# Optimization experiments

Hardware: AMD Instinct MI355X
Metric: run time of the kernel (lower is better)

The kernel has to match this reference:

```python
import jax, jax.numpy as jnp
import numpy as np

N_NODES = 100000
N_EDGES = 1600000
D = 64
L = 3


def setup_inputs() -> dict:
    key = jax.random.key(0)
    ks = jax.random.split(key, 6)
    x = jax.random.normal(ks[0], (N_NODES, D), dtype=jnp.float32)
    edge_index = jax.random.randint(ks[1], (2, N_EDGES), 0, N_NODES, dtype=jnp.int64)
    # Stacked SAGEConv params: lin_l (neighbor branch, with bias), lin_r (root branch, no bias)
    scale = 1.0 / np.sqrt(D)
    Wl = jax.random.normal(ks[2], (L, D, D), dtype=jnp.float32) * scale
    bl = jnp.zeros((L, D), dtype=jnp.float32)
    Wr = jax.random.normal(ks[3], (L, D, D), dtype=jnp.float32) * scale
    return {
        "x": x,
        "Wl": Wl,
        "bl": bl,
        "Wr": Wr,
        "edge_index": edge_index,
        "batch_size": N_NODES,
        "framework": 1,
    }


def reference(x, Wl, bl, Wr, edge_index, batch_size, framework):
    src, dst = edge_index[0], edge_index[1]
    n = x.shape[0]
    # in-degree for mean aggregation; isolated nodes -> divide by 1 (result stays 0)
    deg = jax.ops.segment_sum(jnp.ones((src.shape[0],), dtype=x.dtype), dst, num_segments=n)
    inv_deg = (1.0 / jnp.maximum(deg, 1.0))[:, None]  # [N,1]
    for i in range(Wl.shape[0]):
        msg = x[src]                                              # [E, D] gather
        agg = jax.ops.segment_sum(msg, dst, num_segments=n) * inv_deg  # [N, D] mean
        x = jax.nn.relu(agg @ Wl[i].T + bl[i] + x @ Wr[i].T)
    if framework:
        return x
    return x[:batch_size]
```

## Files before the change

kernel.cpp:

```cpp
#include <hip/hip_runtime.h>
#include <hip/hip_bf16.h>


#define D 64
#define KDIM 128
#define TS 64
#define ASTH 136
#define BSH 8
#define BNODES 256
#define ECHUNK 4096
#define BCAP 4864

typedef unsigned long long u64;
typedef unsigned short u16;
typedef __attribute__((ext_vector_type(8))) short bf16x8;
typedef __attribute__((ext_vector_type(4))) float f32x4;

__device__ inline u16 f2bf(float f) {
    unsigned u = __float_as_uint(f);
    return (u16)((u + 0x7fffu + ((u >> 16) & 1u)) >> 16);
}
__device__ inline void bfx8_to_f(uint4 u, float* f) {
    f[0] = __uint_as_float(u.x << 16); f[1] = __uint_as_float(u.x & 0xffff0000u);
    f[2] = __uint_as_float(u.y << 16); f[3] = __uint_as_float(u.y & 0xffff0000u);
    f[4] = __uint_as_float(u.z << 16); f[5] = __uint_as_float(u.z & 0xffff0000u);
    f[6] = __uint_as_float(u.w << 16); f[7] = __uint_as_float(u.w & 0xffff0000u);
}

__global__ __launch_bounds__(256) void setup_kernel(
    const float* __restrict__ x, u16* __restrict__ xb, int total8,
    const float* __restrict__ Wl, const float* __restrict__ Wr,
    u16* __restrict__ wpk, int wtotal)
{
    int gid = blockIdx.x * 256 + threadIdx.x;
    if (gid < total8) {
        float4 a = *(const float4*)(x + (size_t)gid * 8);
        float4 b = *(const float4*)(x + (size_t)gid * 8 + 4);
        uint4 o;
        o.x = (unsigned)f2bf(a.x) | ((unsigned)f2bf(a.y) << 16);
        o.y = (unsigned)f2bf(a.z) | ((unsigned)f2bf(a.w) << 16);
        o.z = (unsigned)f2bf(b.x) | ((unsigned)f2bf(b.y) << 16);
        o.w = (unsigned)f2bf(b.z) | ((unsigned)f2bf(b.w) << 16);
        *(uint4*)(xb + (size_t)gid * 8) = o;
    } else {
        int idx = gid - total8;
        if (idx < wtotal) {
            int j    = idx & 7;
            int lane = (idx >> 3) & 63;
            int nt   = (idx >> 9) & 3;
            int kt   = (idx >> 11) & 3;
            int l    = idx >> 13;
            int k = kt * 32 + (lane >> 4) * 8 + j;
            int n = nt * 16 + (lane & 15);
            float v = (k < D) ? Wl[((l * D) + n) * D + k]
                              : Wr[((l * D) + n) * D + (k - D)];
            wpk[idx] = f2bf(v);
        }
    }
}


__global__ __launch_bounds__(256) void bin_kernel(
    const int* __restrict__ srcp, const int* __restrict__ dstp,
    int* __restrict__ bcnt, u64* __restrict__ staging,
    int nE, int nb)
{
    __shared__ int hist[512];
    __shared__ int bbase[512];
    int t = threadIdx.x;
    int e0 = blockIdx.x * ECHUNK;
    for (int i = t; i < nb; i += 256) hist[i] = 0;
    __syncthreads();
    int dcache[16];
#pragma unroll
    for (int j = 0; j < 16; ++j) {
        int e = e0 + j * 256 + t;
        int d = (e < nE) ? dstp[e] : -1;
        dcache[j] = d;
        if (d >= 0) atomicAdd(&hist[d >> BSH], 1);
    }
    __syncthreads();
    for (int i = t; i < nb; i += 256) {
        int c = hist[i];
        bbase[i] = (c > 0) ? atomicAdd(&bcnt[i], c) : 0;
        hist[i] = 0;
    }
    __syncthreads();
#pragma unroll
    for (int j = 0; j < 16; ++j) {
        int e = e0 + j * 256 + t;
        int d = dcache[j];
        if (d >= 0) {
            int b = d >> BSH;
            int pos = bbase[b] + atomicAdd(&hist[b], 1);
            u64 rec = ((u64)(unsigned)(d & (BNODES - 1)) << 32) | (unsigned)srcp[e];
            staging[(size_t)b * BCAP + pos] = rec;
        }
    }
}

__global__ __launch_bounds__(256) void bucket_build_kernel(
    const u64* __restrict__ staging, const int* __restrict__ bcnt,
    int* __restrict__ offs, float* __restrict__ inv,
    int* __restrict__ csr, int n, int nb, int E)
{
    __shared__ int hist[BNODES];
    __shared__ int loffs[BNODES + 1];
    __shared__ int cur[BNODES];
    __shared__ int sbase;
    int b = blockIdx.x, t = threadIdx.x;
    int n0 = b << BSH;
    int nodes = min(BNODES, n - n0);
    int cnt = bcnt[b];
    const u64* seg = staging + (size_t)b * BCAP;
    if (t < 64) {
        int partial = 0;
        for (int i = t; i < b; i += 64) partial += bcnt[i];
#pragma unroll
        for (int off = 32; off > 0; off >>= 1) partial += __shfl_xor(partial, off);
        if (t == 0) sbase = partial;
    }
    for (int i = t; i < nodes; i += 256) { hist[i] = 0; cur[i] = 0; }
    __syncthreads();
    int gbase = sbase;
    for (int e = t; e < cnt; e += 256) atomicAdd(&hist[(int)(seg[e] >> 32)], 1);
    __syncthreads();
    if (t < 64) {
        int carry = 0;
        for (int base0 = 0; base0 < nodes; base0 += 64) {
            int i = base0 + t;
            int v = (i < nodes) ? hist[i] : 0;
            int inc = v;
#pragma unroll
            for (int off = 1; off < 64; off <<= 1) {
                int v2 = __shfl_up(inc, off);
                if (t >= off) inc += v2;
            }
            if (i < nodes) loffs[i] = carry + (inc - v);
            carry += __shfl(inc, 63);
        }
        if (t == 0) loffs[nodes] = carry;
    }
    __syncthreads();
    for (int i = t; i < nodes; i += 256) {
        offs[n0 + i] = gbase + loffs[i];
        inv[n0 + i] = 1.0f / fmaxf((float)hist[i], 1.0f);
    }
    if (b == nb - 1 && t == 0) offs[n] = E;
    for (int e = t; e < cnt; e += 256) {
        u64 rec = seg[e];
        int dl = (int)(rec >> 32);
        int sv = (int)(rec & 0xffffffffu);
        int pos = loffs[dl] + atomicAdd(&cur[dl], 1);
        csr[gbase + pos] = sv;
    }
}


template <int WRITE_F32>
__global__ __launch_bounds__(512, 6) void layer_kernel(
    const u16* __restrict__ xin, const int* __restrict__ offs,
    const int* __restrict__ csr, const float* __restrict__ inv,
    const u16* __restrict__ wpk,
    const float* __restrict__ bl,
    void* __restrict__ outp, int n)
{
    __shared__ u16 A[TS * ASTH];
    const int t = threadIdx.x, w = t >> 6, lane = t & 63;
    const int sub = lane >> 3;
    const int fl  = lane & 7;
    const int base = lane & 56;
    const int v0 = blockIdx.x * TS;

    const int r = w * 8 + sub;
    const int v = v0 + r;
    int s = 0, e = 0;
    float scale = 0.f;
    uint4 xv = make_uint4(0, 0, 0, 0);
    if (v < n) {
        s = offs[v];
        e = offs[v + 1];
        scale = inv[v];
        xv = *(const uint4*)(xin + (size_t)v * D + fl * 8);
    }
    float acc[8] = {};
    int idx = 0;
    if (s + fl < e) idx = csr[s + fl];
    while (__any(s < e)) {
        int cnt = e - s;
        cnt = cnt < 0 ? 0 : (cnt > 8 ? 8 : cnt);
        int idxv[8];
#pragma unroll
        for (int j = 0; j < 8; ++j) idxv[j] = __shfl(idx, base + j);
        uint4 rows[8];
#pragma unroll
        for (int j = 0; j < 8; ++j)
            rows[j] = *(const uint4*)(xin + (size_t)idxv[j] * D + fl * 8);
        int s2 = s + 8;
        idx = 0;
        if (s2 + fl < e) idx = csr[s2 + fl];
#pragma unroll
        for (int j = 0; j < 8; ++j) {
            float f[8];
            bfx8_to_f(rows[j], f);
            float m = (j < cnt) ? 1.f : 0.f;
#pragma unroll
            for (int q = 0; q < 8; ++q) acc[q] = fmaf(f[q], m, acc[q]);
        }
        s = s2;
    }
    uint4 o;
    o.x = (unsigned)f2bf(acc[0] * scale) | ((unsigned)f2bf(acc[1] * scale) << 16);
    o.y = (unsigned)f2bf(acc[2] * scale) | ((unsigned)f2bf(acc[3] * scale) << 16);
    o.z = (unsigned)f2bf(acc[4] * scale) | ((unsigned)f2bf(acc[5] * scale) << 16);
    o.w = (unsigned)f2bf(acc[6] * scale) | ((unsigned)f2bf(acc[7] * scale) << 16);
    *(uint4*)(&A[r * ASTH + fl * 8]) = o;
    *(uint4*)(&A[r * ASTH + D + fl * 8]) = xv;
    __syncthreads();

    const int m = lane & 15, quad = lane >> 4;
    const int row16 = (w >> 1) * 16;
    const int ntb = (w & 1) * 2;
    f32x4 cacc[2];
    cacc[0] = (f32x4){0.f, 0.f, 0.f, 0.f};
    cacc[1] = (f32x4){0.f, 0.f, 0.f, 0.f};
#pragma unroll
    for (int kt = 0; kt < 4; ++kt) {
        bf16x8 af = *(const bf16x8*)(&A[(row16 + m) * ASTH + kt * 32 + quad * 8]);
#pragma unroll
        for (int ntl = 0; ntl < 2; ++ntl) {
            bf16x8 bf = *(const bf16x8*)(wpk + (size_t)((kt * 4 + ntb + ntl) * 64 + lane) * 8);
            cacc[ntl] = __builtin_amdgcn_mfma_f32_16x16x32_bf16(af, bf, cacc[ntl], 0, 0, 0);
        }
    }
#pragma unroll
    for (int ntl = 0; ntl < 2; ++ntl) {
        int col = (ntb + ntl) * 16 + m;
        float bias = bl[col];
#pragma unroll
        for (int reg = 0; reg < 4; ++reg) {
            int row = row16 + quad * 4 + reg;
            int vv = v0 + row;
            if (vv < n) {
                float val = fmaxf(cacc[ntl][reg] + bias, 0.f);
                if (WRITE_F32)
                    ((float*)outp)[(size_t)vv * D + col] = val;
                else
                    ((u16*)outp)[(size_t)vv * D + col] = f2bf(val);
            }
        }
    }
}


extern "C" void kernel_launch(void* const* d_in, const int* in_sizes, int n_in,
                              void* d_out, int out_size, void* d_ws, size_t ws_size,
                              hipStream_t stream)
{
    const float* x  = (const float*)d_in[0];
    const float* Wl = (const float*)d_in[1];
    const float* bl = (const float*)d_in[2];
    const float* Wr = (const float*)d_in[3];
    const int*   ei = (const int*)d_in[4];

    const int N = in_sizes[0] / D;
    const int E = in_sizes[4] / 2;
    const int L = in_sizes[1] / (D * D);

    const int* srcp = ei;
    const int* dstp = ei + E;

    const int nbuck = (N + BNODES - 1) >> BSH;

    char* w = (char*)d_ws;
    int* bcnt  = (int*)w;               w += 512 * sizeof(int);
    int* offs  = (int*)w;               w += (size_t)(N + 1) * sizeof(int);
    w = (char*)(((uintptr_t)w + 15) & ~(uintptr_t)15);
    float* inv = (float*)w;             w += (size_t)N * sizeof(float);
    w = (char*)(((uintptr_t)w + 15) & ~(uintptr_t)15);
    int* csr   = (int*)w;               w += (size_t)E * sizeof(int);
    w = (char*)(((uintptr_t)w + 15) & ~(uintptr_t)15);
    u16* wpk   = (u16*)w;               w += (size_t)L * 8192 * sizeof(u16);
    w = (char*)(((uintptr_t)w + 15) & ~(uintptr_t)15);
    u16* xbf0  = (u16*)w;               w += (size_t)N * D * sizeof(u16);
    w = (char*)(((uintptr_t)w + 15) & ~(uintptr_t)15);
    u16* xbf1  = (u16*)w;               w += (size_t)N * D * sizeof(u16);
    w = (char*)(((uintptr_t)w + 15) & ~(uintptr_t)15);
    u16* xbf2  = (u16*)w;               w += (size_t)N * D * sizeof(u16);
    w = (char*)(((uintptr_t)w + 15) & ~(uintptr_t)15);
    u64* staging = (u64*)w;

    hipMemsetAsync(bcnt, 0, 512 * sizeof(int), stream);

    int total8 = N * D / 8;
    int wtotal = L * 8192;
    setup_kernel<<<(total8 + wtotal + 255) / 256, 256, 0, stream>>>(
        x, xbf0, total8, Wl, Wr, wpk, wtotal);
    bin_kernel<<<(E + ECHUNK - 1) / ECHUNK, 256, 0, stream>>>(srcp, dstp, bcnt, staging, E, nbuck);
    bucket_build_kernel<<<nbuck, 256, 0, stream>>>(staging, bcnt, offs, inv, csr, N, nbuck, E);

    const int nblk = (N + TS - 1) / TS;
    const u16* xcur = xbf0;
    for (int i = 0; i < L; ++i) {
        const u16* wpl = wpk + (size_t)i * 8192;
        const float* bll = bl + (size_t)i * D;
        if (i == L - 1) {
            layer_kernel<1><<<nblk, 512, 0, stream>>>(xcur, offs, csr, inv, wpl, bll, d_out, N);
        } else {
            u16* xdst = (i & 1) ? xbf2 : xbf1;
            layer_kernel<0><<<nblk, 512, 0, stream>>>(xcur, offs, csr, inv, wpl, bll, xdst, N);
            xcur = xdst;
        }
    }
}
```

Measured before the change: 290.2 us.

## Sort nodes by in-degree within buckets to balance wavefront gather loops

Bucket build now computes a per-bucket counting sort of nodes by in-degree (capped at 63) and writes a node permutation. The layer kernel processes nodes in permuted order, so each wavefront's eight nodes have similar degree and the `__any` gather loop wastes fewer iterations on divergence. In exchange, the root-row loads and output stores become scattered within a 256-node bucket, and one extra permutation lookup is added per node and per output element.

```diff
diff --git a/kernel.cpp b/kernel.cpp
--- a/kernel.cpp
+++ b/kernel.cpp
@@ -101,12 +101,15 @@
 
 __global__ __launch_bounds__(256) void bucket_build_kernel(
     const u64* __restrict__ staging, const int* __restrict__ bcnt,
-    int* __restrict__ offs, float* __restrict__ inv,
+    int* __restrict__ offs, float* __restrict__ inv, int* __restrict__ perm,
     int* __restrict__ csr, int n, int nb, int E)
 {
     __shared__ int hist[BNODES];
     __shared__ int loffs[BNODES + 1];
     __shared__ int cur[BNODES];
+    __shared__ int dhist[64];
+    __shared__ int dbase[64];
+    __shared__ int dcur[64];
     __shared__ int sbase;
     int b = blockIdx.x, t = threadIdx.x;
     int n0 = b << BSH;
@@ -121,10 +124,12 @@
         if (t == 0) sbase = partial;
     }
     for (int i = t; i < nodes; i += 256) { hist[i] = 0; cur[i] = 0; }
+    if (t < 64) { dhist[t] = 0; dcur[t] = 0; }
     __syncthreads();
     int gbase = sbase;
     for (int e = t; e < cnt; e += 256) atomicAdd(&hist[(int)(seg[e] >> 32)], 1);
     __syncthreads();
+    for (int i = t; i < nodes; i += 256) atomicAdd(&dhist[min(hist[i], 63)], 1);
     if (t < 64) {
         int carry = 0;
         for (int base0 = 0; base0 < nodes; base0 += 64) {
@@ -142,11 +147,27 @@
         if (t == 0) loffs[nodes] = carry;
     }
     __syncthreads();
+    if (t < 64) {
+        int v = dhist[t];
+        int inc = v;
+#pragma unroll
+        for (int off = 1; off < 64; off <<= 1) {
+            int v2 = __shfl_up(inc, off);
+            if (t >= off) inc += v2;
+        }
+        dbase[t] = inc - v;
+    }
     for (int i = t; i < nodes; i += 256) {
         offs[n0 + i] = gbase + loffs[i];
         inv[n0 + i] = 1.0f / fmaxf((float)hist[i], 1.0f);
     }
     if (b == nb - 1 && t == 0) offs[n] = E;
+    __syncthreads();
+    for (int i = t; i < nodes; i += 256) {
+        int bin = min(hist[i], 63);
+        int pos = dbase[bin] + atomicAdd(&dcur[bin], 1);
+        perm[n0 + pos] = n0 + i;
+    }
     for (int e = t; e < cnt; e += 256) {
         u64 rec = seg[e];
         int dl = (int)(rec >> 32);
@@ -161,6 +182,7 @@
 __global__ __launch_bounds__(512, 6) void layer_kernel(
     const u16* __restrict__ xin, const int* __restrict__ offs,
     const int* __restrict__ csr, const float* __restrict__ inv,
+    const int* __restrict__ perm,
     const u16* __restrict__ wpk,
     const float* __restrict__ bl,
     void* __restrict__ outp, int n)
@@ -173,15 +195,15 @@
     const int v0 = blockIdx.x * TS;
 
     const int r = w * 8 + sub;
-    const int v = v0 + r;
     int s = 0, e = 0;
     float scale = 0.f;
     uint4 xv = make_uint4(0, 0, 0, 0);
-    if (v < n) {
-        s = offs[v];
-        e = offs[v + 1];
-        scale = inv[v];
-        xv = *(const uint4*)(xin + (size_t)v * D + fl * 8);
+    if (v0 + r < n) {
+        int pv = perm[v0 + r];
+        s = offs[pv];
+        e = offs[pv + 1];
+        scale = inv[pv];
+        xv = *(const uint4*)(xin + (size_t)pv * D + fl * 8);
     }
     float acc[8] = {};
     int idx = 0;
@@ -240,8 +262,8 @@
 #pragma unroll
         for (int reg = 0; reg < 4; ++reg) {
             int row = row16 + quad * 4 + reg;
-            int vv = v0 + row;
-            if (vv < n) {
+            if (v0 + row < n) {
+                int vv = perm[v0 + row];
                 float val = fmaxf(cacc[ntl][reg] + bias, 0.f);
                 if (WRITE_F32)
                     ((float*)outp)[(size_t)vv * D + col] = val;
@@ -278,6 +300,8 @@
     w = (char*)(((uintptr_t)w + 15) & ~(uintptr_t)15);
     float* inv = (float*)w;             w += (size_t)N * sizeof(float);
     w = (char*)(((uintptr_t)w + 15) & ~(uintptr_t)15);
+    int* perm  = (int*)w;               w += (size_t)N * sizeof(int);
+    w = (char*)(((uintptr_t)w + 15) & ~(uintptr_t)15);
     int* csr   = (int*)w;               w += (size_t)E * sizeof(int);
     w = (char*)(((uintptr_t)w + 15) & ~(uintptr_t)15);
     u16* wpk   = (u16*)w;               w += (size_t)L * 8192 * sizeof(u16);
@@ -297,7 +321,7 @@
     setup_kernel<<<(total8 + wtotal + 255) / 256, 256, 0, stream>>>(
         x, xbf0, total8, Wl, Wr, wpk, wtotal);
     bin_kernel<<<(E + ECHUNK - 1) / ECHUNK, 256, 0, stream>>>(srcp, dstp, bcnt, staging, E, nbuck);
-    bucket_build_kernel<<<nbuck, 256, 0, stream>>>(staging, bcnt, offs, inv, csr, N, nbuck, E);
+    bucket_build_kernel<<<nbuck, 256, 0, stream>>>(staging, bcnt, offs, inv, perm, csr, N, nbuck, E);
 
     const int nblk = (N + TS - 1) / TS;
     const u16* xcur = xbf0;
@@ -305,10 +329,10 @@
         const u16* wpl = wpk + (size_t)i * 8192;
         const float* bll = bl + (size_t)i * D;
         if (i == L - 1) {
-            layer_kernel<1><<<nblk, 512, 0, stream>>>(xcur, offs, csr, inv, wpl, bll, d_out, N);
+            layer_kernel<1><<<nblk, 512, 0, stream>>>(xcur, offs, csr, inv, perm, wpl, bll, d_out, N);
         } else {
             u16* xdst = (i & 1) ? xbf2 : xbf1;
-            layer_kernel<0><<<nblk, 512, 0, stream>>>(xcur, offs, csr, inv, wpl, bll, xdst, N);
+            layer_kernel<0><<<nblk, 512, 0, stream>>>(xcur, offs, csr, inv, perm, wpl, bll, xdst, N);
             xcur = xdst;
         }
     }
```

Result: slower. 323.5 us (+11.5%).
